# Performance work log

Measured on AMD Instinct MI355X. Metric: run time of the kernel, lower is better.

Reference implementation:

```python
import jax, jax.numpy as jnp
from jax import lax
import numpy as np

B, L, C = 16, 4096, 512
G = 8            # n_groups
CG = C // G      # group_dim = 64
WD = 4           # weather_dim
ORF = 10.0       # offset_range_factor


def conv1d(x, w, b=None):
    # x: [N, Cin, L], w: [Cout, Cin, 3], stride 1, padding 1
    y = lax.conv_general_dilated(x, w, window_strides=(1,), padding=[(1, 1)],
                                 dimension_numbers=('NCH', 'OIH', 'NCH'))
    if b is not None:
        y = y + b[None, :, None]
    return y


def group_norm(x, gamma, beta, groups=4, eps=1e-5):
    N, Cc, Ln = x.shape
    xr = x.reshape(N, groups, Cc // groups, Ln)
    mu = xr.mean(axis=(2, 3), keepdims=True)
    var = ((xr - mu) ** 2).mean(axis=(2, 3), keepdims=True)
    xn = ((xr - mu) / jnp.sqrt(var + eps)).reshape(N, Cc, Ln)
    return xn * gamma[None, :, None] + beta[None, :, None]


def grid_sample_bilinear_border(inp, grid):
    # Faithful torch F.grid_sample(mode='bilinear', padding_mode='border', align_corners=True)
    # inp: [N, C, H, W]; grid: [N, Ho, Wo, 2], grid[...,0]=x (width coord), grid[...,1]=y (height coord)
    N, Cc, H, W = inp.shape
    _, Ho, Wo, _ = grid.shape
    gx, gy = grid[..., 0], grid[..., 1]
    ix = jnp.clip((gx + 1.0) * 0.5 * (W - 1), 0.0, W - 1)  # border padding clamps coords
    iy = jnp.clip((gy + 1.0) * 0.5 * (H - 1), 0.0, H - 1)
    ix0f = jnp.floor(ix); iy0f = jnp.floor(iy)
    wx = ix - ix0f; wy = iy - iy0f
    ix0 = jnp.clip(ix0f.astype(jnp.int32), 0, W - 1)
    iy0 = jnp.clip(iy0f.astype(jnp.int32), 0, H - 1)
    ix1 = jnp.clip(ix0 + 1, 0, W - 1)
    iy1 = jnp.clip(iy0 + 1, 0, H - 1)
    flat = inp.reshape(N, Cc, H * W)
    def gather(iyk, ixk):
        idx = (iyk * W + ixk).reshape(N, 1, Ho * Wo)
        return jnp.take_along_axis(flat, idx, axis=2).reshape(N, Cc, Ho, Wo)
    v00 = gather(iy0, ix0); v01 = gather(iy0, ix1)
    v10 = gather(iy1, ix0); v11 = gather(iy1, ix1)
    wx = wx[:, None, :, :]; wy = wy[:, None, :, :]
    return (v00 * (1 - wy) * (1 - wx) + v01 * (1 - wy) * wx
            + v10 * wy * (1 - wx) + v11 * wy * wx)


def _forward(x, x_ext, w1, b1, gn_g, gn_b, w2, b2, w3, gate):
    xt = jnp.transpose(x, (0, 2, 1))              # [B, C, L]
    xg = xt.reshape(B * G, CG, L)                 # [B*G, CG, L]
    xe = jnp.transpose(x_ext, (0, 2, 1))          # [B, WD, L]
    xe = jnp.tile(xe, (G, 1, 1))                  # torch .repeat(n_groups,1,1)
    pin = jnp.concatenate([xg, xe], axis=1)       # [B*G, CG+WD, L]
    h = jax.nn.gelu(group_norm(conv1d(pin, w1, b1), gn_g, gn_b), approximate=False)
    h = jax.nn.gelu(conv1d(h, w2, b2), approximate=False)
    offset = jnp.tanh(conv1d(h, w3)) * ORF        # [B*G, 1, L]
    off_n = offset * (2.0 / (L - 1.0))
    ref = (jnp.linspace(0.5, L - 0.5, L, dtype=x.dtype) / (L - 1.0)) * 2.0 - 1.0
    grid_x = jnp.clip(ref[None, None, :, None] + off_n[..., None], -1.0, 1.0)  # [B*G,1,L,1]
    grid = jnp.concatenate([grid_x, jnp.zeros_like(grid_x)], axis=-1)
    grid = jnp.transpose(grid, (0, 2, 1, 3))      # [B*G, L, 1, 2]
    xs = grid_sample_bilinear_border(xg[..., None], grid)[..., 0]  # [B*G, CG, L]
    x_out = xg + jnp.tanh(gate) * xs
    x_out = x_out.reshape(B, C, L)
    return jnp.transpose(x_out, (0, 2, 1)), offset


def setup_inputs() -> dict:
    key = jax.random.key(0)
    ks = jax.random.split(key, 8)
    s = 0.05
    return {
        'x': jax.random.normal(ks[0], (B, L, C), jnp.float32),
        'x_ext': jax.random.normal(ks[1], (B, L, WD), jnp.float32),
        'w1': jax.random.normal(ks[2], (64, CG + WD, 3), jnp.float32) * s,
        'b1': jax.random.normal(ks[3], (64,), jnp.float32) * s,
        'gn_g': jnp.ones((64,), jnp.float32),
        'gn_b': jnp.zeros((64,), jnp.float32),
        'w2': jax.random.normal(ks[4], (32, 64, 3), jnp.float32) * s,
        'b2': jax.random.normal(ks[5], (32,), jnp.float32) * s,
        'w3': jax.random.normal(ks[6], (1, 32, 3), jnp.float32) * s,
        'gate': jnp.array([0.5], jnp.float32),
    }


def reference(x, x_ext, w1, b1, gn_g, gn_b, w2, b2, w3, gate):
    return _forward(x, x_ext, w1, b1, gn_g, gn_b, w2, b2, w3, gate)
```

## Files before the change

### kernel.cpp

```cpp
#include <hip/hip_runtime.h>
#include <hip/hip_bf16.h>

#define BB 16
#define LL 4096
#define CC 512
#define NG 128
#define IC1 68
#define OC1 64
#define OC2 32

typedef short short8 __attribute__((ext_vector_type(8)));
typedef float f32x4 __attribute__((ext_vector_type(4)));

__device__ inline ushort f2b(float f) {
    __hip_bfloat16 h = __float2bfloat16(f);
    return *reinterpret_cast<ushort*>(&h);
}
__device__ inline float b2f(ushort u) {
    __hip_bfloat16 h;
    *reinterpret_cast<ushort*>(&h) = u;
    return __bfloat162float(h);
}
__device__ inline float fast_tanh(float y) {
    float e = __expf(2.0f * y);
    return 1.0f - 2.0f / (e + 1.0f);
}
__device__ inline float fast_gelu(float x) {
    float y = x * (0.7978845608f + 0.0356774081f * x * x);
    return 0.5f * x * (1.0f + fast_tanh(y));
}

__global__ __launch_bounds__(256) void k_prep(const float* __restrict__ x,
    const float* __restrict__ w1, const float* __restrict__ w2,
    const float* __restrict__ gate,
    ushort* __restrict__ w1b, ushort* __restrict__ w2b, float* __restrict__ corr)
{
    int idx = blockIdx.x * 256 + threadIdx.x;
    if (idx < 18432) {
        int k = idx / 6144; int r = idx - k * 6144;
        int oc = r / 96;    int icp = r - oc * 96;
        float v = (icp < IC1) ? w1[(oc * IC1 + icp) * 3 + k] : 0.0f;
        w1b[idx] = f2b(v);
    } else if (idx < 24576) {
        int j = idx - 18432;
        int k = j / 2048; int r = j - k * 2048;
        int oc = r / 64;  int ic = r - oc * 64;
        w2b[j] = f2b(w2[(oc * OC1 + ic) * 3 + k]);
    } else if (idx < 32768) {
        int i3 = idx - 24576;
        int b = i3 >> 9; int ch = i3 & 511;
        float tg = tanhf(gate[0]);
        corr[i3] = tg * 0.5f *
            (x[((size_t)(b * LL + 2047)) * CC + ch] +
             x[((size_t)(b * LL + 2048)) * CC + ch]);
    }
}

#define K1_ROWS 130
#define K1_STR  104
__global__ __launch_bounds__(256) void k1_conv1(const float* __restrict__ x,
    const float* __restrict__ xe, const float* __restrict__ b1,
    const ushort* __restrict__ w1b, const float* __restrict__ corr,
    ushort* __restrict__ h1, float* __restrict__ part, float* __restrict__ out)
{
    __shared__ ushort pin[K1_ROWS * K1_STR];
    const int n = blockIdx.y, lt = blockIdx.x;
    const int b = n >> 3, g = n & 7, be = n & 15;
    const int l0 = lt * 128;
    const int t = threadIdx.x;

    {
        const int q = t & 15;
        const float4 corrv = *(const float4*)&corr[(b << 9) + g * 64 + q * 4];
        for (int pos = t; pos < K1_ROWS * 16; pos += 256) {
            int li = pos >> 4;
            int l = l0 - 1 + li;
            float4 v = make_float4(0.f, 0.f, 0.f, 0.f);
            if (l >= 0 && l < LL) {
                v = *(const float4*)&x[((size_t)(b * LL + l)) * CC + g * 64 + q * 4];
                if (li >= 1 && li <= 128) {
                    float4 o;
                    o.x = v.x + corrv.x; o.y = v.y + corrv.y;
                    o.z = v.z + corrv.z; o.w = v.w + corrv.w;
                    *(float4*)&out[((size_t)(b * LL + l)) * CC + g * 64 + q * 4] = o;
                }
            }
            uint lo = (uint)f2b(v.x) | ((uint)f2b(v.y) << 16);
            uint hi = (uint)f2b(v.z) | ((uint)f2b(v.w) << 16);
            *(uint2*)&pin[li * K1_STR + q * 4] = make_uint2(lo, hi);
        }
    }
    for (int li = t; li < K1_ROWS; li += 256) {
        int l = l0 - 1 + li;
        float4 v = make_float4(0.f, 0.f, 0.f, 0.f);
        if (l >= 0 && l < LL)
            v = *(const float4*)&xe[(size_t)(be * LL + l) * 4];
        uint lo = (uint)f2b(v.x) | ((uint)f2b(v.y) << 16);
        uint hi = (uint)f2b(v.z) | ((uint)f2b(v.w) << 16);
        *(uint2*)&pin[li * K1_STR + 64] = make_uint2(lo, hi);
    }
    {
        uint* pz = (uint*)pin;
        for (int pos = t; pos < K1_ROWS * 14; pos += 256) {
            int li = pos / 14, j = pos - li * 14;
            pz[li * 52 + 34 + j] = 0u;
        }
    }
    __syncthreads();

    const int lane = t & 63;
    const int w = t >> 6;
    const int och = w & 1, lh = w >> 1;
    const int m = lane & 15, h = lane >> 4;

    short8 fa[2][9];
#pragma unroll
    for (int mi = 0; mi < 2; ++mi)
#pragma unroll
        for (int k = 0; k < 3; ++k)
#pragma unroll
            for (int c = 0; c < 3; ++c)
                fa[mi][k * 3 + c] = *(const short8*)&w1b[
                    (size_t)(k * 64 + och * 32 + mi * 16 + m) * 96 + c * 32 + h * 8];

    f32x4 acc[2][4] = {};
#pragma unroll
    for (int tt = 0; tt < 4; ++tt) {
        const int rowbase = lh * 64 + tt * 16 + m;
#pragma unroll
        for (int k = 0; k < 3; ++k) {
#pragma unroll
            for (int c = 0; c < 3; ++c) {
                short8 fb = *(const short8*)&pin[(rowbase + k) * K1_STR + c * 32 + h * 8];
                acc[0][tt] = __builtin_amdgcn_mfma_f32_16x16x32_bf16(fa[0][k * 3 + c], fb, acc[0][tt], 0, 0, 0);
                acc[1][tt] = __builtin_amdgcn_mfma_f32_16x16x32_bf16(fa[1][k * 3 + c], fb, acc[1][tt], 0, 0, 0);
            }
        }
    }

#pragma unroll
    for (int mi = 0; mi < 2; ++mi) {
        float bias[4];
#pragma unroll
        for (int r = 0; r < 4; ++r)
            bias[r] = b1[och * 32 + mi * 16 + h * 4 + r];
        float s1 = 0.f, s2 = 0.f;
#pragma unroll
        for (int tt = 0; tt < 4; ++tt) {
            int l = l0 + lh * 64 + tt * 16 + m;
            float v0 = acc[mi][tt][0] + bias[0];
            float v1 = acc[mi][tt][1] + bias[1];
            float v2 = acc[mi][tt][2] + bias[2];
            float v3 = acc[mi][tt][3] + bias[3];
            s1 += v0 + v1 + v2 + v3;
            s2 += v0 * v0 + v1 * v1 + v2 * v2 + v3 * v3;
            uint2 pk;
            pk.x = (uint)f2b(v0) | ((uint)f2b(v1) << 16);
            pk.y = (uint)f2b(v2) | ((uint)f2b(v3) << 16);
            *(uint2*)&h1[((size_t)n * LL + l) * 64 + och * 32 + mi * 16 + h * 4] = pk;
        }
#pragma unroll
        for (int off = 32; off > 0; off >>= 1) {
            s1 += __shfl_down(s1, off, 64);
            s2 += __shfl_down(s2, off, 64);
        }
        if (lane == 0) {
            int gidx = och * 2 + mi;
            part[(((size_t)n * 4 + gidx) * 64 + lt * 2 + lh) * 2 + 0] = s1;
            part[(((size_t)n * 4 + gidx) * 64 + lt * 2 + lh) * 2 + 1] = s2;
        }
    }
}

#define K3_ROWS 130
#define K3_STR  72
#define H2_STR  132
__global__ __launch_bounds__(256) void k3_rest(const ushort* __restrict__ h1,
    const float* __restrict__ part, const float* __restrict__ gn_g,
    const float* __restrict__ gn_b, const float* __restrict__ b2,
    const ushort* __restrict__ w2b, const float* __restrict__ w3,
    float* __restrict__ offs)
{
    __shared__ ushort p2[K3_ROWS * K3_STR];
    __shared__ float h2s[OC2 * H2_STR];
    __shared__ float sstats[8];
    const int n = blockIdx.y, lt = blockIdx.x;
    const int l0 = lt * 126;
    const int t = threadIdx.x;
    const int lane = t & 63;
    const int w = t >> 6;

    {
        float2 p = *(const float2*)&part[(((size_t)n * 4 + w) * 64 + lane) * 2];
        float s1 = p.x, s2 = p.y;
#pragma unroll
        for (int off = 32; off > 0; off >>= 1) {
            s1 += __shfl_down(s1, off, 64);
            s2 += __shfl_down(s2, off, 64);
        }
        if (lane == 0) {
            float mean = s1 * (1.0f / 65536.0f);
            float var  = s2 * (1.0f / 65536.0f) - mean * mean;
            sstats[w * 2 + 0] = mean;
            sstats[w * 2 + 1] = 1.0f / sqrtf(var + 1e-5f);
        }
    }
    __syncthreads();

    const int q = t & 7;
    float Af[8], Bf[8];
    {
        int gi = q >> 1;
        float mean = sstats[gi * 2], istd = sstats[gi * 2 + 1];
#pragma unroll
        for (int j = 0; j < 8; ++j) {
            float ga = gn_g[q * 8 + j];
            Af[j] = istd * ga;
            Bf[j] = gn_b[q * 8 + j] - mean * Af[j];
        }
    }

    for (int pos = t; pos < K3_ROWS * 8; pos += 256) {
        int li = pos >> 3;
        int l = l0 - 2 + li;
        uint4 o = make_uint4(0u, 0u, 0u, 0u);
        if (l >= 0 && l < LL) {
            uint4 u = *(const uint4*)&h1[((size_t)n * LL + l) * 64 + q * 8];
            const ushort* us = (const ushort*)&u;
            ushort vb[8];
#pragma unroll
            for (int j = 0; j < 8; ++j) {
                float xn = fmaf(b2f(us[j]), Af[j], Bf[j]);
                vb[j] = f2b(fast_gelu(xn));
            }
            o.x = (uint)vb[0] | ((uint)vb[1] << 16);
            o.y = (uint)vb[2] | ((uint)vb[3] << 16);
            o.z = (uint)vb[4] | ((uint)vb[5] << 16);
            o.w = (uint)vb[6] | ((uint)vb[7] << 16);
        }
        *(uint4*)&p2[li * K3_STR + q * 8] = o;
    }
    __syncthreads();

    const int m = lane & 15, h = lane >> 4;

    short8 fa[2][6];
#pragma unroll
    for (int mi = 0; mi < 2; ++mi)
#pragma unroll
        for (int k = 0; k < 3; ++k)
#pragma unroll
            for (int c = 0; c < 2; ++c)
                fa[mi][k * 2 + c] = *(const short8*)&w2b[
                    (size_t)(k * 32 + mi * 16 + m) * 64 + c * 32 + h * 8];

    float bias2[2][4];
#pragma unroll
    for (int mi = 0; mi < 2; ++mi)
#pragma unroll
        for (int r = 0; r < 4; ++r)
            bias2[mi][r] = b2[mi * 16 + h * 4 + r];

    f32x4 acc[2][2] = {};
#pragma unroll
    for (int u = 0; u < 2; ++u) {
        const int jb = (w * 2 + u) * 16 + m;
#pragma unroll
        for (int k = 0; k < 3; ++k) {
#pragma unroll
            for (int c = 0; c < 2; ++c) {
                short8 fb = *(const short8*)&p2[(jb + k) * K3_STR + c * 32 + h * 8];
                acc[0][u] = __builtin_amdgcn_mfma_f32_16x16x32_bf16(fa[0][k * 2 + c], fb, acc[0][u], 0, 0, 0);
                acc[1][u] = __builtin_amdgcn_mfma_f32_16x16x32_bf16(fa[1][k * 2 + c], fb, acc[1][u], 0, 0, 0);
            }
        }
    }
#pragma unroll
    for (int mi = 0; mi < 2; ++mi) {
#pragma unroll
        for (int u = 0; u < 2; ++u) {
            int j = (w * 2 + u) * 16 + m;
            int lj = l0 - 1 + j;
#pragma unroll
            for (int r = 0; r < 4; ++r) {
                int oc = mi * 16 + h * 4 + r;
                float v = 0.f;
                if (lj >= 0 && lj < LL)
                    v = fast_gelu(acc[mi][u][r] + bias2[mi][r]);
                h2s[oc * H2_STR + j] = v;
            }
        }
    }
    __syncthreads();

    for (int qq = t; qq < 126; qq += 256) {
        int l = l0 + qq;
        if (l >= LL) break;
        float a = 0.f;
#pragma unroll
        for (int ic = 0; ic < OC2; ++ic) {
            a = fmaf(w3[ic * 3 + 0], h2s[ic * H2_STR + qq],     a);
            a = fmaf(w3[ic * 3 + 1], h2s[ic * H2_STR + qq + 1], a);
            a = fmaf(w3[ic * 3 + 2], h2s[ic * H2_STR + qq + 2], a);
        }
        offs[(size_t)n * LL + l] = fast_tanh(a) * 10.0f;
    }
}

extern "C" void kernel_launch(void* const* d_in, const int* in_sizes, int n_in,
                              void* d_out, int out_size, void* d_ws, size_t ws_size,
                              hipStream_t stream)
{
    const float* x    = (const float*)d_in[0];
    const float* xext = (const float*)d_in[1];
    const float* w1   = (const float*)d_in[2];
    const float* b1   = (const float*)d_in[3];
    const float* gng  = (const float*)d_in[4];
    const float* gnb  = (const float*)d_in[5];
    const float* w2   = (const float*)d_in[6];
    const float* b2   = (const float*)d_in[7];
    const float* w3   = (const float*)d_in[8];
    const float* gate = (const float*)d_in[9];

    float* out  = (float*)d_out;
    float* offs = out + (size_t)BB * LL * CC;

    char* ws = (char*)d_ws;
    ushort* h1  = (ushort*)(ws);
    float* part = (float*)(ws + 67108864);
    ushort* w1b = (ushort*)(ws + 67371008);
    ushort* w2b = (ushort*)(ws + 67407872);
    float* corr = (float*)(ws + 67420160);

    k_prep<<<128, 256, 0, stream>>>(x, w1, w2, gate, w1b, w2b, corr);
    dim3 g1(32, NG);
    k1_conv1<<<g1, 256, 0, stream>>>(x, xext, b1, w1b, corr, h1, part, out);
    dim3 g3(33, NG);
    k3_rest<<<g3, 256, 0, stream>>>(h1, part, gng, gnb, b2, w2b, w3, offs);
}
```

Measured before the change: 156.1 us.

## Recompute conv1 in fused kernel instead of storing h1 intermediate

The first pass now only computes conv1 to gather GroupNorm partial sums and no longer writes the bf16 h1 tensor or the residual output. A new fused kernel reloads x with a 3-row halo, recomputes conv1 with MFMA, and applies GroupNorm (with conv1's bias folded in) and GELU straight into shared memory. It then runs conv2 and conv3, and writes both the output and the offsets. This removes the h1 round-trip through global memory, but x is read twice, conv1 runs twice, and the tile shrinks to 124 rows, so there are more blocks and more halo overhead.

```diff
diff --git a/kernel.cpp b/kernel.cpp
--- a/kernel.cpp
+++ b/kernel.cpp
@@ -58,10 +58,9 @@
 
 #define K1_ROWS 130
 #define K1_STR  104
-__global__ __launch_bounds__(256) void k1_conv1(const float* __restrict__ x,
+__global__ __launch_bounds__(256) void ka_stats(const float* __restrict__ x,
     const float* __restrict__ xe, const float* __restrict__ b1,
-    const ushort* __restrict__ w1b, const float* __restrict__ corr,
-    ushort* __restrict__ h1, float* __restrict__ part, float* __restrict__ out)
+    const ushort* __restrict__ w1b, float* __restrict__ part)
 {
     __shared__ ushort pin[K1_ROWS * K1_STR];
     const int n = blockIdx.y, lt = blockIdx.x;
@@ -71,20 +70,12 @@
 
     {
         const int q = t & 15;
-        const float4 corrv = *(const float4*)&corr[(b << 9) + g * 64 + q * 4];
         for (int pos = t; pos < K1_ROWS * 16; pos += 256) {
             int li = pos >> 4;
             int l = l0 - 1 + li;
             float4 v = make_float4(0.f, 0.f, 0.f, 0.f);
-            if (l >= 0 && l < LL) {
+            if (l >= 0 && l < LL)
                 v = *(const float4*)&x[((size_t)(b * LL + l)) * CC + g * 64 + q * 4];
-                if (li >= 1 && li <= 128) {
-                    float4 o;
-                    o.x = v.x + corrv.x; o.y = v.y + corrv.y;
-                    o.z = v.z + corrv.z; o.w = v.w + corrv.w;
-                    *(float4*)&out[((size_t)(b * LL + l)) * CC + g * 64 + q * 4] = o;
-                }
-            }
             uint lo = (uint)f2b(v.x) | ((uint)f2b(v.y) << 16);
             uint hi = (uint)f2b(v.z) | ((uint)f2b(v.w) << 16);
             *(uint2*)&pin[li * K1_STR + q * 4] = make_uint2(lo, hi);
@@ -147,17 +138,12 @@
         float s1 = 0.f, s2 = 0.f;
 #pragma unroll
         for (int tt = 0; tt < 4; ++tt) {
-            int l = l0 + lh * 64 + tt * 16 + m;
             float v0 = acc[mi][tt][0] + bias[0];
             float v1 = acc[mi][tt][1] + bias[1];
             float v2 = acc[mi][tt][2] + bias[2];
             float v3 = acc[mi][tt][3] + bias[3];
             s1 += v0 + v1 + v2 + v3;
             s2 += v0 * v0 + v1 * v1 + v2 * v2 + v3 * v3;
-            uint2 pk;
-            pk.x = (uint)f2b(v0) | ((uint)f2b(v1) << 16);
-            pk.y = (uint)f2b(v2) | ((uint)f2b(v3) << 16);
-            *(uint2*)&h1[((size_t)n * LL + l) * 64 + och * 32 + mi * 16 + h * 4] = pk;
         }
 #pragma unroll
         for (int off = 32; off > 0; off >>= 1) {
@@ -172,20 +158,25 @@
     }
 }
 
-#define K3_ROWS 130
-#define K3_STR  72
-#define H2_STR  132
-__global__ __launch_bounds__(256) void k3_rest(const ushort* __restrict__ h1,
-    const float* __restrict__ part, const float* __restrict__ gn_g,
-    const float* __restrict__ gn_b, const float* __restrict__ b2,
-    const ushort* __restrict__ w2b, const float* __restrict__ w3,
-    float* __restrict__ offs)
+#define BT 124
+#define XR 130
+#define P2R 130
+#define P2STR 72
+#define H2STR 132
+__global__ __launch_bounds__(256) void kb_fused(const float* __restrict__ x,
+    const float* __restrict__ xe, const float* __restrict__ b1,
+    const ushort* __restrict__ w1b, const float* __restrict__ part,
+    const float* __restrict__ gn_g, const float* __restrict__ gn_b,
+    const float* __restrict__ b2, const ushort* __restrict__ w2b,
+    const float* __restrict__ w3, const float* __restrict__ corr,
+    float* __restrict__ out, float* __restrict__ offs)
 {
-    __shared__ ushort p2[K3_ROWS * K3_STR];
-    __shared__ float h2s[OC2 * H2_STR];
+    __shared__ ushort pin[XR * K1_STR];
+    __shared__ ushort p2[P2R * P2STR];
     __shared__ float sstats[8];
     const int n = blockIdx.y, lt = blockIdx.x;
-    const int l0 = lt * 126;
+    const int b = n >> 3, g = n & 7, be = n & 15;
+    const int l0 = lt * BT;
     const int t = threadIdx.x;
     const int lane = t & 63;
     const int w = t >> 6;
@@ -205,53 +196,113 @@
             sstats[w * 2 + 1] = 1.0f / sqrtf(var + 1e-5f);
         }
     }
+
+    {
+        const int q = t & 15;
+        const float4 corrv = *(const float4*)&corr[(b << 9) + g * 64 + q * 4];
+        for (int pos = t; pos < XR * 16; pos += 256) {
+            int li = pos >> 4;
+            int l = l0 - 3 + li;
+            float4 v = make_float4(0.f, 0.f, 0.f, 0.f);
+            if (l >= 0 && l < LL) {
+                v = *(const float4*)&x[((size_t)(b * LL + l)) * CC + g * 64 + q * 4];
+                if (li >= 3 && li < 3 + BT) {
+                    float4 o;
+                    o.x = v.x + corrv.x; o.y = v.y + corrv.y;
+                    o.z = v.z + corrv.z; o.w = v.w + corrv.w;
+                    *(float4*)&out[((size_t)(b * LL + l)) * CC + g * 64 + q * 4] = o;
+                }
+            }
+            uint lo = (uint)f2b(v.x) | ((uint)f2b(v.y) << 16);
+            uint hi = (uint)f2b(v.z) | ((uint)f2b(v.w) << 16);
+            *(uint2*)&pin[li * K1_STR + q * 4] = make_uint2(lo, hi);
+        }
+        for (int li = t; li < XR; li += 256) {
+            int l = l0 - 3 + li;
+            float4 v = make_float4(0.f, 0.f, 0.f, 0.f);
+            if (l >= 0 && l < LL)
+                v = *(const float4*)&xe[(size_t)(be * LL + l) * 4];
+            uint lo = (uint)f2b(v.x) | ((uint)f2b(v.y) << 16);
+            uint hi = (uint)f2b(v.z) | ((uint)f2b(v.w) << 16);
+            *(uint2*)&pin[li * K1_STR + 64] = make_uint2(lo, hi);
+        }
+        uint* pz = (uint*)pin;
+        for (int pos = t; pos < XR * 14; pos += 256) {
+            int li = pos / 14, j = pos - li * 14;
+            pz[li * 52 + 34 + j] = 0u;
+        }
+        uint* qz = (uint*)p2;
+        for (int i = t; i < 72; i += 256)
+            qz[128 * 36 + i] = 0u;
+    }
     __syncthreads();
 
-    const int q = t & 7;
-    float Af[8], Bf[8];
-    {
-        int gi = q >> 1;
+    const int och = w & 1, lh = w >> 1;
+    const int m = lane & 15, h = lane >> 4;
+
+    short8 fa[2][9];
+#pragma unroll
+    for (int mi = 0; mi < 2; ++mi)
+#pragma unroll
+        for (int k = 0; k < 3; ++k)
+#pragma unroll
+            for (int c = 0; c < 3; ++c)
+                fa[mi][k * 3 + c] = *(const short8*)&w1b[
+                    (size_t)(k * 64 + och * 32 + mi * 16 + m) * 96 + c * 32 + h * 8];
+
+    f32x4 acc[2][4] = {};
+#pragma unroll
+    for (int tt = 0; tt < 4; ++tt) {
+        const int rowbase = lh * 64 + tt * 16 + m;
+#pragma unroll
+        for (int k = 0; k < 3; ++k) {
+#pragma unroll
+            for (int c = 0; c < 3; ++c) {
+                short8 fb = *(const short8*)&pin[(rowbase + k) * K1_STR + c * 32 + h * 8];
+                acc[0][tt] = __builtin_amdgcn_mfma_f32_16x16x32_bf16(fa[0][k * 3 + c], fb, acc[0][tt], 0, 0, 0);
+                acc[1][tt] = __builtin_amdgcn_mfma_f32_16x16x32_bf16(fa[1][k * 3 + c], fb, acc[1][tt], 0, 0, 0);
+            }
+        }
+    }
+
+#pragma unroll
+    for (int mi = 0; mi < 2; ++mi) {
+        int gi = och * 2 + mi;
         float mean = sstats[gi * 2], istd = sstats[gi * 2 + 1];
-#pragma unroll
-        for (int j = 0; j < 8; ++j) {
-            float ga = gn_g[q * 8 + j];
-            Af[j] = istd * ga;
-            Bf[j] = gn_b[q * 8 + j] - mean * Af[j];
-        }
-    }
-
-    for (int pos = t; pos < K3_ROWS * 8; pos += 256) {
-        int li = pos >> 3;
-        int l = l0 - 2 + li;
-        uint4 o = make_uint4(0u, 0u, 0u, 0u);
-        if (l >= 0 && l < LL) {
-            uint4 u = *(const uint4*)&h1[((size_t)n * LL + l) * 64 + q * 8];
-            const ushort* us = (const ushort*)&u;
-            ushort vb[8];
-#pragma unroll
-            for (int j = 0; j < 8; ++j) {
-                float xn = fmaf(b2f(us[j]), Af[j], Bf[j]);
-                vb[j] = f2b(fast_gelu(xn));
-            }
-            o.x = (uint)vb[0] | ((uint)vb[1] << 16);
-            o.y = (uint)vb[2] | ((uint)vb[3] << 16);
-            o.z = (uint)vb[4] | ((uint)vb[5] << 16);
-            o.w = (uint)vb[6] | ((uint)vb[7] << 16);
-        }
-        *(uint4*)&p2[li * K3_STR + q * 8] = o;
+        float A_[4], B_[4];
+#pragma unroll
+        for (int r = 0; r < 4; ++r) {
+            int oc = och * 32 + mi * 16 + h * 4 + r;
+            float ga = gn_g[oc];
+            A_[r] = istd * ga;
+            B_[r] = gn_b[oc] + (b1[oc] - mean) * A_[r];
+        }
+#pragma unroll
+        for (int tt = 0; tt < 4; ++tt) {
+            int p = lh * 64 + tt * 16 + m;
+            int l = l0 - 2 + p;
+            uint2 pk = make_uint2(0u, 0u);
+            if (l >= 0 && l < LL) {
+                float v0 = fast_gelu(fmaf(acc[mi][tt][0], A_[0], B_[0]));
+                float v1 = fast_gelu(fmaf(acc[mi][tt][1], A_[1], B_[1]));
+                float v2 = fast_gelu(fmaf(acc[mi][tt][2], A_[2], B_[2]));
+                float v3 = fast_gelu(fmaf(acc[mi][tt][3], A_[3], B_[3]));
+                pk.x = (uint)f2b(v0) | ((uint)f2b(v1) << 16);
+                pk.y = (uint)f2b(v2) | ((uint)f2b(v3) << 16);
+            }
+            *(uint2*)&p2[p * P2STR + och * 32 + mi * 16 + h * 4] = pk;
+        }
     }
     __syncthreads();
 
-    const int m = lane & 15, h = lane >> 4;
-
-    short8 fa[2][6];
+    short8 fa2[2][6];
 #pragma unroll
     for (int mi = 0; mi < 2; ++mi)
 #pragma unroll
         for (int k = 0; k < 3; ++k)
 #pragma unroll
             for (int c = 0; c < 2; ++c)
-                fa[mi][k * 2 + c] = *(const short8*)&w2b[
+                fa2[mi][k * 2 + c] = *(const short8*)&w2b[
                     (size_t)(k * 32 + mi * 16 + m) * 64 + c * 32 + h * 8];
 
     float bias2[2][4];
@@ -261,7 +312,7 @@
         for (int r = 0; r < 4; ++r)
             bias2[mi][r] = b2[mi * 16 + h * 4 + r];
 
-    f32x4 acc[2][2] = {};
+    f32x4 acc2[2][2] = {};
 #pragma unroll
     for (int u = 0; u < 2; ++u) {
         const int jb = (w * 2 + u) * 16 + m;
@@ -269,12 +320,13 @@
         for (int k = 0; k < 3; ++k) {
 #pragma unroll
             for (int c = 0; c < 2; ++c) {
-                short8 fb = *(const short8*)&p2[(jb + k) * K3_STR + c * 32 + h * 8];
-                acc[0][u] = __builtin_amdgcn_mfma_f32_16x16x32_bf16(fa[0][k * 2 + c], fb, acc[0][u], 0, 0, 0);
-                acc[1][u] = __builtin_amdgcn_mfma_f32_16x16x32_bf16(fa[1][k * 2 + c], fb, acc[1][u], 0, 0, 0);
-            }
-        }
-    }
+                short8 fb = *(const short8*)&p2[(jb + k) * P2STR + c * 32 + h * 8];
+                acc2[0][u] = __builtin_amdgcn_mfma_f32_16x16x32_bf16(fa2[0][k * 2 + c], fb, acc2[0][u], 0, 0, 0);
+                acc2[1][u] = __builtin_amdgcn_mfma_f32_16x16x32_bf16(fa2[1][k * 2 + c], fb, acc2[1][u], 0, 0, 0);
+            }
+        }
+    }
+    float* h2s = (float*)pin;
 #pragma unroll
     for (int mi = 0; mi < 2; ++mi) {
 #pragma unroll
@@ -286,22 +338,22 @@
                 int oc = mi * 16 + h * 4 + r;
                 float v = 0.f;
                 if (lj >= 0 && lj < LL)
-                    v = fast_gelu(acc[mi][u][r] + bias2[mi][r]);
-                h2s[oc * H2_STR + j] = v;
+                    v = fast_gelu(acc2[mi][u][r] + bias2[mi][r]);
+                h2s[oc * H2STR + j] = v;
             }
         }
     }
     __syncthreads();
 
-    for (int qq = t; qq < 126; qq += 256) {
+    for (int qq = t; qq < BT; qq += 256) {
         int l = l0 + qq;
         if (l >= LL) break;
         float a = 0.f;
 #pragma unroll
         for (int ic = 0; ic < OC2; ++ic) {
-            a = fmaf(w3[ic * 3 + 0], h2s[ic * H2_STR + qq],     a);
-            a = fmaf(w3[ic * 3 + 1], h2s[ic * H2_STR + qq + 1], a);
-            a = fmaf(w3[ic * 3 + 2], h2s[ic * H2_STR + qq + 2], a);
+            a = fmaf(w3[ic * 3 + 0], h2s[ic * H2STR + qq],     a);
+            a = fmaf(w3[ic * 3 + 1], h2s[ic * H2STR + qq + 1], a);
+            a = fmaf(w3[ic * 3 + 2], h2s[ic * H2STR + qq + 2], a);
         }
         offs[(size_t)n * LL + l] = fast_tanh(a) * 10.0f;
     }
@@ -326,15 +378,15 @@
     float* offs = out + (size_t)BB * LL * CC;
 
     char* ws = (char*)d_ws;
-    ushort* h1  = (ushort*)(ws);
-    float* part = (float*)(ws + 67108864);
-    ushort* w1b = (ushort*)(ws + 67371008);
-    ushort* w2b = (ushort*)(ws + 67407872);
-    float* corr = (float*)(ws + 67420160);
+    float* part = (float*)(ws);
+    ushort* w1b = (ushort*)(ws + 262144);
+    ushort* w2b = (ushort*)(ws + 299008);
+    float* corr = (float*)(ws + 311296);
 
     k_prep<<<128, 256, 0, stream>>>(x, w1, w2, gate, w1b, w2b, corr);
     dim3 g1(32, NG);
-    k1_conv1<<<g1, 256, 0, stream>>>(x, xext, b1, w1b, corr, h1, part, out);
-    dim3 g3(33, NG);
-    k3_rest<<<g3, 256, 0, stream>>>(h1, part, gng, gnb, b2, w2b, w3, offs);
-}
+    ka_stats<<<g1, 256, 0, stream>>>(x, xext, b1, w1b, part);
+    dim3 g3(34, NG);
+    kb_fused<<<g3, 256, 0, stream>>>(x, xext, b1, w1b, part, gng, gnb, b2, w2b,
+                                     w3, corr, out, offs);
+}
```

Result: slower. 161.3 us (+3.3%).
